# Kernel tuning notes

Hardware: AMD Instinct MI355X
Metric: run time of the kernel (lower is better)

The kernel has to match this reference:

```python
import jax, jax.numpy as jnp
import numpy as np

MAX_SEQ_LEN = 4096

def bigbird_block_rand_mask(from_seq_length, to_seq_length, from_block_size, to_block_size, num_rand_blocks, last_idx=-1):
    rand_attn = np.zeros((from_seq_length // from_block_size - 2, num_rand_blocks), dtype=np.int32)
    middle_seq = np.arange(1, to_seq_length // to_block_size - 1, dtype=np.int32)
    last = to_seq_length // to_block_size - 1
    if last_idx > 2 * to_block_size:
        last = last_idx // to_block_size - 1
    r = num_rand_blocks
    nfb = from_seq_length // from_block_size
    for i in range(1, nfb - 1):
        start = i - 2
        end = i
        if i == 1:
            rand_attn[i - 1, :] = np.random.permutation(middle_seq[2:last])[:r]
        elif i == 2:
            rand_attn[i - 1, :] = np.random.permutation(middle_seq[3:last])[:r]
        elif i == nfb - 3:
            rand_attn[i - 1, :] = np.random.permutation(middle_seq[:last])[:r]
        elif i == nfb - 2:
            rand_attn[i - 1, :] = np.random.permutation(middle_seq[:last])[:r]
        elif start > last:
            start = last
            rand_attn[i - 1, :] = np.random.permutation(middle_seq[:start])[:r]
        elif end + 1 == last:
            rand_attn[i - 1, :] = np.random.permutation(middle_seq[:start])[:r]
        else:
            rand_attn[i - 1, :] = np.random.permutation(np.concatenate((middle_seq[:start], middle_seq[end + 1:last])))[:r]
    return rand_attn

def full_bigbird_mask(from_seq_length, to_seq_length, from_block_size, to_block_size, rand_attn):
    attn_mask = np.zeros((MAX_SEQ_LEN, MAX_SEQ_LEN), dtype=np.int32)
    for i in range(1, from_seq_length // from_block_size - 1):
        attn_mask[i * from_block_size:(i + 1) * from_block_size, (i - 1) * to_block_size:(i + 2) * to_block_size] = 1
        for j in rand_attn[i - 1, :]:
            attn_mask[i * from_block_size:(i + 1) * from_block_size, j * to_block_size:(j + 1) * to_block_size] = 1
    attn_mask[:from_block_size, :] = 1
    attn_mask[:, :to_block_size] = 1
    attn_mask[:, -to_block_size:] = 1
    attn_mask[-from_block_size:, :] = 1
    return attn_mask[:from_seq_length, :to_seq_length].astype(bool)

def setup_inputs() -> dict:
    B, H, F, T, D = 2, 16, 1024, 1024, 64
    BS, R, SEED = 64, 3, 0
    np.random.seed(SEED)
    rand_attn = np.stack([
        bigbird_block_rand_mask(MAX_SEQ_LEN, MAX_SEQ_LEN, BS, BS, R, last_idx=1024)[:F // BS - 2]
        for _ in range(H)
    ], axis=0)
    mask = np.stack([full_bigbird_mask(F, T, BS, BS, rand_attn[h]) for h in range(H)], axis=0)
    attention_mask = jnp.asarray(mask[None].astype(np.float32))  # [1, H, F, T]
    key = jax.random.key(0)
    kq, kk, kv = jax.random.split(key, 3)
    return {
        'query_layer': jax.random.normal(kq, (B, H, F, D), dtype=jnp.float32),
        'key_layer': jax.random.normal(kk, (B, H, T, D), dtype=jnp.float32),
        'value_layer': jax.random.normal(kv, (B, H, T, D), dtype=jnp.float32),
        'attention_mask': attention_mask,
    }

def reference(query_layer, key_layer, value_layer, attention_mask):
    d = query_layer.shape[-1]
    scores = jnp.einsum('bnfh,bnth->bnft', query_layer, key_layer) * (1.0 / np.sqrt(float(d)))
    scores = scores + (1.0 - attention_mask) * -10000.0
    probs = jax.nn.softmax(scores, axis=-1)
    # [batch, from_seq, heads, size_per_head]
    return jnp.einsum('bnft,bnth->bfnh', probs, value_layer)
```

## Files before the change

### kernel.cpp

```cpp
#include <hip/hip_runtime.h>

typedef __attribute__((ext_vector_type(4))) float f32x4;
typedef __attribute__((ext_vector_type(8))) short bf16x8;
typedef _Float16 f16x8 __attribute__((ext_vector_type(8)));

#define MFMA16(a, b, c) __builtin_amdgcn_mfma_f32_16x16x32_f16((a), (b), (c), 0, 0, 0)
#define MFMABF(a, b, c) __builtin_amdgcn_mfma_f32_16x16x32_bf16((a), (b), (c), 0, 0, 0)

constexpr size_t TILE_FRAG_BYTES = 8192;
constexpr size_t NTILES = 512;
constexpr size_t ARR_S  = NTILES * TILE_FRAG_BYTES;
constexpr size_t WS_NEED = 2 * ARR_S;

__device__ __forceinline__ int swz_off(int row, int col) {
    return (row * 128 + col * 2) ^ ((row & 7) << 4);
}
__device__ __forceinline__ f16x8 ld_frag16(const char* tile, int row, int col) {
    return *(const f16x8*)(tile + swz_off(row, col));
}

__global__ __launch_bounds__(256) void bigbird_prepass(
    const float* __restrict__ K, const float* __restrict__ V,
    char* __restrict__ ws) {
    __shared__ float kf[64][66];
    __shared__ float vf[64][66];
    const int tile = blockIdx.x;
    const int tid  = threadIdx.x;
    const int row  = tid >> 2;
    const int c0   = (tid & 3) << 4;
    const float* Kt = K + (size_t)tile * 4096;
    const float* Vt = V + (size_t)tile * 4096;
    {
        const float* p = Kt + row * 64 + c0;
        f32x4 a = *(const f32x4*)p, bq = *(const f32x4*)(p + 4),
              c = *(const f32x4*)(p + 8), d = *(const f32x4*)(p + 12);
#pragma unroll
        for (int e = 0; e < 4; ++e) {
            kf[row][c0 + e] = a[e];      kf[row][c0 + 4 + e] = bq[e];
            kf[row][c0 + 8 + e] = c[e];  kf[row][c0 + 12 + e] = d[e];
        }
        const float* q = Vt + row * 64 + c0;
        f32x4 e0 = *(const f32x4*)q, e1 = *(const f32x4*)(q + 4),
              e2 = *(const f32x4*)(q + 8), e3 = *(const f32x4*)(q + 12);
#pragma unroll
        for (int e = 0; e < 4; ++e) {
            vf[row][c0 + e] = e0[e];     vf[row][c0 + 4 + e] = e1[e];
            vf[row][c0 + 8 + e] = e2[e]; vf[row][c0 + 12 + e] = e3[e];
        }
    }
    __syncthreads();
    f16x8* Ko = (f16x8*)(ws + (size_t)tile * TILE_FRAG_BYTES);
    f16x8* Vo = (f16x8*)(ws + ARR_S + (size_t)tile * TILE_FRAG_BYTES);
#pragma unroll
    for (int t = 0; t < 2; ++t) {
        int s = tid + t * 256;
        int f = s >> 6, lane = s & 63;
        int j = f >> 1, kk = f & 1;
        int l16 = lane & 15, g = lane >> 4;
        f16x8 kv, vv;
#pragma unroll
        for (int e = 0; e < 8; ++e) {
            kv[e] = (_Float16)kf[j * 16 + l16][kk * 32 + g * 8 + e];
            vv[e] = (_Float16)vf[kk * 32 + g * 8 + e][j * 16 + l16];
        }
        Ko[s] = kv;
        Vo[s] = vv;
    }
}

__global__ __launch_bounds__(256) void bigbird_main(
    const float* __restrict__ Q, const float* __restrict__ M,
    const char* __restrict__ ws, float* __restrict__ Out) {
    constexpr int H = 16, F = 1024, D = 64;

    __shared__ char p_sm[8192];
    __shared__ int flags[16];
    __shared__ int list[16];
    __shared__ int ncnt;

    const int i0  = blockIdx.x;
    const int xcd = i0 & 7;
    const int q0  = i0 >> 3;
    const int grp = xcd * 4 + (q0 >> 4);
    const int fb  = q0 & 15;
    const int b   = grp >> 4;
    const int h   = grp & 15;
    const int bh  = grp;

    const int tid  = threadIdx.x;
    const int lane = tid & 63;
    const int w    = tid >> 6;
    const int g    = lane >> 4;
    const int l16  = lane & 15;

    if (tid < 16)
        flags[tid] = (M[((size_t)(h * 1024 + fb * 64)) * 1024 + tid * 64] > 0.5f) ? 1 : 0;

    f16x8 qf[2];
    {
        const float* qr = Q + ((size_t)bh * F + fb * 64 + w * 16 + l16) * D;
#pragma unroll
        for (int kk = 0; kk < 2; ++kk) {
            const float* p = qr + kk * 32 + g * 8;
            f32x4 a = *(const f32x4*)p;
            f32x4 c = *(const f32x4*)(p + 4);
#pragma unroll
            for (int e = 0; e < 8; ++e)
                qf[kk][e] = (_Float16)((e < 4 ? a[e] : c[e - 4]) * 0.125f);
        }
    }
    __syncthreads();
    if (tid == 0) {
        int nn = 0;
        for (int t = 0; t < 16; ++t)
            if (flags[t]) list[nn++] = t;
        ncnt = nn;
    }
    __syncthreads();
    const int n = ncnt;

    f32x4 acc[4];
    float m_r[4], l_r[4];
#pragma unroll
    for (int j = 0; j < 4; ++j) acc[j] = f32x4{0.f, 0.f, 0.f, 0.f};
#pragma unroll
    for (int r = 0; r < 4; ++r) { m_r[r] = -1e30f; l_r[r] = 0.f; }

    const f16x8* Kbase = (const f16x8*)ws + (size_t)bh * 16 * 512;
    const f16x8* Vbase = (const f16x8*)(ws + ARR_S) + (size_t)bh * 16 * 512;

    for (int i = 0; i < n; ++i) {
        const int tb = list[i];
        const f16x8* Kf = Kbase + (size_t)tb * 512;
        const f16x8* Vf = Vbase + (size_t)tb * 512;

        f16x8 kfr[4][2], vfr[4][2];
#pragma unroll
        for (int j = 0; j < 4; ++j)
#pragma unroll
            for (int kk = 0; kk < 2; ++kk) {
                kfr[j][kk] = Kf[(j * 2 + kk) * 64 + lane];
                vfr[j][kk] = Vf[(j * 2 + kk) * 64 + lane];
            }

        f32x4 s[4];
#pragma unroll
        for (int j = 0; j < 4; ++j) {
            s[j] = f32x4{0.f, 0.f, 0.f, 0.f};
#pragma unroll
            for (int kk = 0; kk < 2; ++kk)
                s[j] = MFMA16(qf[kk], kfr[j][kk], s[j]);
        }

        float rmax[4];
#pragma unroll
        for (int r = 0; r < 4; ++r)
            rmax[r] = fmaxf(fmaxf(s[0][r], s[1][r]), fmaxf(s[2][r], s[3][r]));
#pragma unroll
        for (int off = 1; off < 16; off <<= 1)
#pragma unroll
            for (int r = 0; r < 4; ++r)
                rmax[r] = fmaxf(rmax[r], __shfl_xor(rmax[r], off, 64));
        float alpha[4], psum[4];
#pragma unroll
        for (int r = 0; r < 4; ++r) {
            float mn = fmaxf(m_r[r], rmax[r]);
            alpha[r] = __expf(m_r[r] - mn);
            m_r[r]   = mn;
            psum[r]  = 0.f;
        }
#pragma unroll
        for (int j = 0; j < 4; ++j)
#pragma unroll
            for (int r = 0; r < 4; ++r) {
                float pe = __expf(s[j][r] - m_r[r]);
                s[j][r] = pe;
                psum[r] += pe;
            }
#pragma unroll
        for (int off = 1; off < 16; off <<= 1)
#pragma unroll
            for (int r = 0; r < 4; ++r)
                psum[r] += __shfl_xor(psum[r], off, 64);
#pragma unroll
        for (int r = 0; r < 4; ++r)
            l_r[r] = l_r[r] * alpha[r] + psum[r];
#pragma unroll
        for (int j = 0; j < 4; ++j)
#pragma unroll
            for (int r = 0; r < 4; ++r)
                acc[j][r] *= alpha[r];

#pragma unroll
        for (int j = 0; j < 4; ++j)
#pragma unroll
            for (int r = 0; r < 4; ++r) {
                int row = w * 16 + g * 4 + r;
                *(_Float16*)(p_sm + swz_off(row, j * 16 + l16)) = (_Float16)s[j][r];
            }
        asm volatile("s_waitcnt lgkmcnt(0)" ::: "memory");
        __builtin_amdgcn_sched_barrier(0);

#pragma unroll
        for (int kk = 0; kk < 2; ++kk) {
            f16x8 pa = ld_frag16(p_sm, w * 16 + l16, kk * 32 + g * 8);
#pragma unroll
            for (int jd = 0; jd < 4; ++jd)
                acc[jd] = MFMA16(pa, vfr[jd][kk], acc[jd]);
        }
    }

#pragma unroll
    for (int r = 0; r < 4; ++r) {
        float inv = 1.0f / l_r[r];
        int f = fb * 64 + w * 16 + g * 4 + r;
        float* ob = Out + ((size_t)(b * F + f) * H + h) * D;
#pragma unroll
        for (int jd = 0; jd < 4; ++jd)
            ob[jd * 16 + l16] = acc[jd][r] * inv;
    }
}

__device__ __forceinline__ unsigned short f2bf(float x) {
    unsigned u = __builtin_bit_cast(unsigned, x);
    unsigned r = u + 0x7fffu + ((u >> 16) & 1u);
    return (unsigned short)(r >> 16);
}
__device__ __forceinline__ float bf2f(unsigned short h) {
    return __builtin_bit_cast(float, (unsigned)h << 16);
}
__device__ __forceinline__ bf16x8 ld_fragb(const char* tile, int row, int col) {
    return *(const bf16x8*)(tile + swz_off(row, col));
}
__device__ __forceinline__ void stage_rm_fb(const float* __restrict__ src,
                                            char* hi_t, char* lo_t, float scale) {
    const int tid = threadIdx.x;
    const int row = tid >> 2;
    const int c0  = (tid & 3) << 4;
    const float* p = src + row * 64 + c0;
    f32x4 vv[4] = { *(const f32x4*)(p), *(const f32x4*)(p + 4),
                    *(const f32x4*)(p + 8), *(const f32x4*)(p + 12) };
    bf16x8 h2[2], l2[2];
#pragma unroll
    for (int e = 0; e < 16; ++e) {
        float x = vv[e >> 2][e & 3] * scale;
        unsigned short hb = f2bf(x);
        unsigned short lb = f2bf(x - bf2f(hb));
        h2[e >> 3][e & 7] = (short)hb;
        l2[e >> 3][e & 7] = (short)lb;
    }
#pragma unroll
    for (int gi = 0; gi < 2; ++gi) {
        int off = swz_off(row, c0 + gi * 8);
        *(bf16x8*)(hi_t + off) = h2[gi];
        *(bf16x8*)(lo_t + off) = l2[gi];
    }
}
__device__ __forceinline__ void stage_tr_fb(const float* __restrict__ src,
                                            char* hi_t, char* lo_t) {
    const int tid = threadIdx.x;
    const int t  = tid >> 2;
    const int c0 = (tid & 3) << 4;
    const float* p = src + t * 64 + c0;
    f32x4 vv[4] = { *(const f32x4*)(p), *(const f32x4*)(p + 4),
                    *(const f32x4*)(p + 8), *(const f32x4*)(p + 12) };
#pragma unroll
    for (int e = 0; e < 16; ++e) {
        float x = vv[e >> 2][e & 3];
        unsigned short hb = f2bf(x);
        unsigned short lb = f2bf(x - bf2f(hb));
        int d = c0 + e;
        int off = (d * 128 + t * 2) ^ ((d & 7) << 4);
        *(unsigned short*)(hi_t + off) = hb;
        *(unsigned short*)(lo_t + off) = lb;
    }
}
__global__ __launch_bounds__(256) void bigbird_kernel_fb(
    const float* __restrict__ Q, const float* __restrict__ K,
    const float* __restrict__ V, const float* __restrict__ M,
    float* __restrict__ Out) {
    constexpr int H = 16, F = 1024, D = 64;
    __shared__ char kq_hi[8192];
    __shared__ char kq_lo[8192];
    __shared__ char vt_hi[8192];
    __shared__ char vt_lo[8192];
    __shared__ char p_sm[8192];
    __shared__ int flags[16];
    const int bid = blockIdx.x;
    const int fb  = bid & 15;
    const int h   = (bid >> 4) & 15;
    const int b   = bid >> 8;
    const int tid  = threadIdx.x;
    const int lane = tid & 63;
    const int w    = tid >> 6;
    const int g    = lane >> 4;
    const int l16  = lane & 15;
    if (tid < 16)
        flags[tid] = (M[(h * 1024 + fb * 64) * 1024 + tid * 64] > 0.5f) ? 1 : 0;
    const float* qb = Q + ((size_t)(b * H + h) * F + fb * 64) * D;
    stage_rm_fb(qb, kq_hi, kq_lo, 0.125f);
    __syncthreads();
    bf16x8 qh[2], ql[2];
#pragma unroll
    for (int kk = 0; kk < 2; ++kk) {
        qh[kk] = ld_fragb(kq_hi, w * 16 + l16, kk * 32 + g * 8);
        ql[kk] = ld_fragb(kq_lo, w * 16 + l16, kk * 32 + g * 8);
    }
    f32x4 acc[4];
    float m_r[4], l_r[4];
#pragma unroll
    for (int j = 0; j < 4; ++j) acc[j] = f32x4{0.f, 0.f, 0.f, 0.f};
#pragma unroll
    for (int r = 0; r < 4; ++r) { m_r[r] = -1e30f; l_r[r] = 0.f; }
    const float* kb = K + (size_t)(b * H + h) * 1024 * D;
    const float* vb = V + (size_t)(b * H + h) * 1024 * D;
    for (int tb = 0; tb < 16; ++tb) {
        if (!flags[tb]) continue;
        __syncthreads();
        stage_rm_fb(kb + tb * 64 * D, kq_hi, kq_lo, 1.0f);
        stage_tr_fb(vb + tb * 64 * D, vt_hi, vt_lo);
        __syncthreads();
        f32x4 s[4];
#pragma unroll
        for (int j = 0; j < 4; ++j) {
            s[j] = f32x4{0.f, 0.f, 0.f, 0.f};
#pragma unroll
            for (int kk = 0; kk < 2; ++kk) {
                bf16x8 bhf = ld_fragb(kq_hi, j * 16 + l16, kk * 32 + g * 8);
                bf16x8 blf = ld_fragb(kq_lo, j * 16 + l16, kk * 32 + g * 8);
                s[j] = MFMABF(qh[kk], bhf, s[j]);
                s[j] = MFMABF(qh[kk], blf, s[j]);
                s[j] = MFMABF(ql[kk], bhf, s[j]);
            }
        }
        float rmax[4];
#pragma unroll
        for (int r = 0; r < 4; ++r)
            rmax[r] = fmaxf(fmaxf(s[0][r], s[1][r]), fmaxf(s[2][r], s[3][r]));
#pragma unroll
        for (int off = 1; off < 16; off <<= 1)
#pragma unroll
            for (int r = 0; r < 4; ++r)
                rmax[r] = fmaxf(rmax[r], __shfl_xor(rmax[r], off, 64));
        float alpha[4], psum[4];
#pragma unroll
        for (int r = 0; r < 4; ++r) {
            float mn = fmaxf(m_r[r], rmax[r]);
            alpha[r] = __expf(m_r[r] - mn);
            m_r[r]   = mn;
            psum[r]  = 0.f;
        }
#pragma unroll
        for (int j = 0; j < 4; ++j)
#pragma unroll
            for (int r = 0; r < 4; ++r) {
                float pe = __expf(s[j][r] - m_r[r]);
                s[j][r] = pe;
                psum[r] += pe;
            }
#pragma unroll
        for (int off = 1; off < 16; off <<= 1)
#pragma unroll
            for (int r = 0; r < 4; ++r)
                psum[r] += __shfl_xor(psum[r], off, 64);
#pragma unroll
        for (int r = 0; r < 4; ++r)
            l_r[r] = l_r[r] * alpha[r] + psum[r];
#pragma unroll
        for (int j = 0; j < 4; ++j)
#pragma unroll
            for (int r = 0; r < 4; ++r)
                acc[j][r] *= alpha[r];
#pragma unroll
        for (int j = 0; j < 4; ++j)
#pragma unroll
            for (int r = 0; r < 4; ++r) {
                int row = w * 16 + g * 4 + r;
                *(unsigned short*)(p_sm + swz_off(row, j * 16 + l16)) = f2bf(s[j][r]);
            }
        __syncthreads();
#pragma unroll
        for (int kk = 0; kk < 2; ++kk) {
            bf16x8 pa = ld_fragb(p_sm, w * 16 + l16, kk * 32 + g * 8);
#pragma unroll
            for (int jd = 0; jd < 4; ++jd) {
                bf16x8 vh = ld_fragb(vt_hi, jd * 16 + l16, kk * 32 + g * 8);
                bf16x8 vl = ld_fragb(vt_lo, jd * 16 + l16, kk * 32 + g * 8);
                acc[jd] = MFMABF(pa, vh, acc[jd]);
                acc[jd] = MFMABF(pa, vl, acc[jd]);
            }
        }
    }
#pragma unroll
    for (int r = 0; r < 4; ++r) {
        float inv = 1.0f / l_r[r];
        int f = fb * 64 + w * 16 + g * 4 + r;
        float* ob = Out + ((size_t)(b * F + f) * H + h) * D;
#pragma unroll
        for (int jd = 0; jd < 4; ++jd)
            ob[jd * 16 + l16] = acc[jd][r] * inv;
    }
}

extern "C" void kernel_launch(void* const* d_in, const int* in_sizes, int n_in,
                              void* d_out, int out_size, void* d_ws, size_t ws_size,
                              hipStream_t stream) {
    const float* q = (const float*)d_in[0];
    const float* k = (const float*)d_in[1];
    const float* v = (const float*)d_in[2];
    const float* m = (const float*)d_in[3];
    float* out = (float*)d_out;
    if (ws_size >= WS_NEED) {
        bigbird_prepass<<<dim3(512), dim3(256), 0, stream>>>(k, v, (char*)d_ws);
        bigbird_main<<<dim3(512), dim3(256), 0, stream>>>(q, m, (const char*)d_ws, out);
    } else {
        bigbird_kernel_fb<<<dim3(512), dim3(256), 0, stream>>>(q, k, v, m, out);
    }
}
```

Before: 39.00 us.

## Split key blocks across wave pairs with split-softmax merge and smaller query tiles

The main kernel now handles 32 query rows per block instead of 64 and launches twice as many blocks. Within a block, two wave pairs each process alternate key blocks from the sparse list. Their partial softmax states are merged through shared memory with max and sum rescaling before the output is written. The prepass reads K fragments directly from global memory and only stages V through LDS for the transpose. This is meant to raise parallelism and occupancy for a small grid, at the cost of extra LDS traffic and two more barriers for the merge.

Result: no change. 39.08 us (+0.2%).

```diff
diff --git a/kernel.cpp b/kernel.cpp
--- a/kernel.cpp
+++ b/kernel.cpp
@@ -22,58 +22,66 @@
 __global__ __launch_bounds__(256) void bigbird_prepass(
     const float* __restrict__ K, const float* __restrict__ V,
     char* __restrict__ ws) {
-    __shared__ float kf[64][66];
     __shared__ float vf[64][66];
     const int tile = blockIdx.x;
     const int tid  = threadIdx.x;
-    const int row  = tid >> 2;
-    const int c0   = (tid & 3) << 4;
     const float* Kt = K + (size_t)tile * 4096;
     const float* Vt = V + (size_t)tile * 4096;
+    f16x8* Ko = (f16x8*)(ws + (size_t)tile * TILE_FRAG_BYTES);
+    f16x8* Vo = (f16x8*)(ws + ARR_S + (size_t)tile * TILE_FRAG_BYTES);
+
     {
-        const float* p = Kt + row * 64 + c0;
-        f32x4 a = *(const f32x4*)p, bq = *(const f32x4*)(p + 4),
-              c = *(const f32x4*)(p + 8), d = *(const f32x4*)(p + 12);
-#pragma unroll
-        for (int e = 0; e < 4; ++e) {
-            kf[row][c0 + e] = a[e];      kf[row][c0 + 4 + e] = bq[e];
-            kf[row][c0 + 8 + e] = c[e];  kf[row][c0 + 12 + e] = d[e];
-        }
-        const float* q = Vt + row * 64 + c0;
-        f32x4 e0 = *(const f32x4*)q, e1 = *(const f32x4*)(q + 4),
-              e2 = *(const f32x4*)(q + 8), e3 = *(const f32x4*)(q + 12);
+        const int row = tid >> 2;
+        const int c0  = (tid & 3) << 4;
+        const float* p = Vt + row * 64 + c0;
+        f32x4 e0 = *(const f32x4*)p,       e1 = *(const f32x4*)(p + 4),
+              e2 = *(const f32x4*)(p + 8), e3 = *(const f32x4*)(p + 12);
 #pragma unroll
         for (int e = 0; e < 4; ++e) {
             vf[row][c0 + e] = e0[e];     vf[row][c0 + 4 + e] = e1[e];
             vf[row][c0 + 8 + e] = e2[e]; vf[row][c0 + 12 + e] = e3[e];
         }
     }
-    __syncthreads();
-    f16x8* Ko = (f16x8*)(ws + (size_t)tile * TILE_FRAG_BYTES);
-    f16x8* Vo = (f16x8*)(ws + ARR_S + (size_t)tile * TILE_FRAG_BYTES);
 #pragma unroll
     for (int t = 0; t < 2; ++t) {
         int s = tid + t * 256;
         int f = s >> 6, lane = s & 63;
         int j = f >> 1, kk = f & 1;
         int l16 = lane & 15, g = lane >> 4;
-        f16x8 kv, vv;
-#pragma unroll
-        for (int e = 0; e < 8; ++e) {
-            kv[e] = (_Float16)kf[j * 16 + l16][kk * 32 + g * 8 + e];
+        const float* p = Kt + (j * 16 + l16) * 64 + kk * 32 + g * 8;
+        f32x4 a = *(const f32x4*)p;
+        f32x4 c = *(const f32x4*)(p + 4);
+        f16x8 kv;
+#pragma unroll
+        for (int e = 0; e < 4; ++e) {
+            kv[e]     = (_Float16)a[e];
+            kv[4 + e] = (_Float16)c[e];
+        }
+        Ko[s] = kv;
+    }
+    __syncthreads();
+#pragma unroll
+    for (int t = 0; t < 2; ++t) {
+        int s = tid + t * 256;
+        int f = s >> 6, lane = s & 63;
+        int j = f >> 1, kk = f & 1;
+        int l16 = lane & 15, g = lane >> 4;
+        f16x8 vv;
+#pragma unroll
+        for (int e = 0; e < 8; ++e)
             vv[e] = (_Float16)vf[kk * 32 + g * 8 + e][j * 16 + l16];
-        }
-        Ko[s] = kv;
         Vo[s] = vv;
     }
 }
 
-__global__ __launch_bounds__(256) void bigbird_main(
+__global__ __launch_bounds__(256, 4) void bigbird_main(
     const float* __restrict__ Q, const float* __restrict__ M,
     const char* __restrict__ ws, float* __restrict__ Out) {
     constexpr int H = 16, F = 1024, D = 64;
 
-    __shared__ char p_sm[8192];
+    __shared__ char  p_sm[4][2048];
+    __shared__ float O_sm[32][65];
+    __shared__ float m_sm[2][32], l_sm[2][32];
     __shared__ int flags[16];
     __shared__ int list[16];
     __shared__ int ncnt;
@@ -81,8 +89,8 @@
     const int i0  = blockIdx.x;
     const int xcd = i0 & 7;
     const int q0  = i0 >> 3;
-    const int grp = xcd * 4 + (q0 >> 4);
-    const int fb  = q0 & 15;
+    const int grp = xcd * 4 + (q0 >> 5);
+    const int sb  = q0 & 31;
     const int b   = grp >> 4;
     const int h   = grp & 15;
     const int bh  = grp;
@@ -90,15 +98,17 @@
     const int tid  = threadIdx.x;
     const int lane = tid & 63;
     const int w    = tid >> 6;
+    const int ws_  = w & 1;
+    const int wt   = w >> 1;
     const int g    = lane >> 4;
     const int l16  = lane & 15;
 
     if (tid < 16)
-        flags[tid] = (M[((size_t)(h * 1024 + fb * 64)) * 1024 + tid * 64] > 0.5f) ? 1 : 0;
+        flags[tid] = (M[((size_t)(h * 1024 + sb * 32)) * 1024 + tid * 64] > 0.5f) ? 1 : 0;
 
     f16x8 qf[2];
     {
-        const float* qr = Q + ((size_t)bh * F + fb * 64 + w * 16 + l16) * D;
+        const float* qr = Q + ((size_t)bh * F + sb * 32 + ws_ * 16 + l16) * D;
 #pragma unroll
         for (int kk = 0; kk < 2; ++kk) {
             const float* p = qr + kk * 32 + g * 8;
@@ -128,8 +138,9 @@
 
     const f16x8* Kbase = (const f16x8*)ws + (size_t)bh * 16 * 512;
     const f16x8* Vbase = (const f16x8*)(ws + ARR_S) + (size_t)bh * 16 * 512;
-
-    for (int i = 0; i < n; ++i) {
+    char* pw = p_sm[w];
+
+    for (int i = wt; i < n; i += 2) {
         const int tb = list[i];
         const f16x8* Kf = Kbase + (size_t)tb * 512;
         const f16x8* Vf = Vbase + (size_t)tb * 512;
@@ -194,30 +205,69 @@
 #pragma unroll
         for (int j = 0; j < 4; ++j)
 #pragma unroll
-            for (int r = 0; r < 4; ++r) {
-                int row = w * 16 + g * 4 + r;
-                *(_Float16*)(p_sm + swz_off(row, j * 16 + l16)) = (_Float16)s[j][r];
-            }
+            for (int r = 0; r < 4; ++r)
+                *(_Float16*)(pw + swz_off(g * 4 + r, j * 16 + l16)) = (_Float16)s[j][r];
         asm volatile("s_waitcnt lgkmcnt(0)" ::: "memory");
         __builtin_amdgcn_sched_barrier(0);
 
 #pragma unroll
         for (int kk = 0; kk < 2; ++kk) {
-            f16x8 pa = ld_frag16(p_sm, w * 16 + l16, kk * 32 + g * 8);
+            f16x8 pa = ld_frag16(pw, l16, kk * 32 + g * 8);
 #pragma unroll
             for (int jd = 0; jd < 4; ++jd)
                 acc[jd] = MFMA16(pa, vfr[jd][kk], acc[jd]);
         }
     }
 
+    if (l16 == 0) {
+#pragma unroll
+        for (int r = 0; r < 4; ++r) {
+            int row = ws_ * 16 + g * 4 + r;
+            m_sm[wt][row] = m_r[r];
+            l_sm[wt][row] = l_r[r];
+        }
+    }
+    __syncthreads();
+    float inv_l[4];
 #pragma unroll
     for (int r = 0; r < 4; ++r) {
-        float inv = 1.0f / l_r[r];
-        int f = fb * 64 + w * 16 + g * 4 + r;
+        int row = ws_ * 16 + g * 4 + r;
+        float m0 = m_sm[0][row], m1 = m_sm[1][row];
+        float mm = fmaxf(m0, m1);
+        float ll = l_sm[0][row] * __expf(m0 - mm) + l_sm[1][row] * __expf(m1 - mm);
+        inv_l[r] = 1.0f / ll;
+        float sc = __expf(m_r[r] - mm);
+#pragma unroll
+        for (int j = 0; j < 4; ++j) acc[j][r] *= sc;
+    }
+    if (wt == 0) {
+#pragma unroll
+        for (int j = 0; j < 4; ++j)
+#pragma unroll
+            for (int r = 0; r < 4; ++r)
+                O_sm[ws_ * 16 + g * 4 + r][j * 16 + l16] = acc[j][r];
+    }
+    __syncthreads();
+    if (wt == 1) {
+#pragma unroll
+        for (int j = 0; j < 4; ++j)
+#pragma unroll
+            for (int r = 0; r < 4; ++r)
+                O_sm[ws_ * 16 + g * 4 + r][j * 16 + l16] += acc[j][r];
+    }
+    __syncthreads();
+
+#pragma unroll
+    for (int r = 0; r < 4; ++r) {
+        int row = ws_ * 16 + g * 4 + r;
+        int f = sb * 32 + row;
+        float inv = inv_l[r];
         float* ob = Out + ((size_t)(b * F + f) * H + h) * D;
 #pragma unroll
-        for (int jd = 0; jd < 4; ++jd)
-            ob[jd * 16 + l16] = acc[jd][r] * inv;
+        for (int j2 = 0; j2 < 2; ++j2) {
+            int col = wt * 32 + j2 * 16 + l16;
+            ob[col] = O_sm[row][col] * inv;
+        }
     }
 }
 
@@ -284,7 +334,7 @@
     __shared__ char kq_lo[8192];
     __shared__ char vt_hi[8192];
     __shared__ char vt_lo[8192];
-    __shared__ char p_sm[8192];
+    __shared__ char p_smf[8192];
     __shared__ int flags[16];
     const int bid = blockIdx.x;
     const int fb  = bid & 15;
@@ -376,12 +426,12 @@
 #pragma unroll
             for (int r = 0; r < 4; ++r) {
                 int row = w * 16 + g * 4 + r;
-                *(unsigned short*)(p_sm + swz_off(row, j * 16 + l16)) = f2bf(s[j][r]);
+                *(unsigned short*)(p_smf + swz_off(row, j * 16 + l16)) = f2bf(s[j][r]);
             }
         __syncthreads();
 #pragma unroll
         for (int kk = 0; kk < 2; ++kk) {
-            bf16x8 pa = ld_fragb(p_sm, w * 16 + l16, kk * 32 + g * 8);
+            bf16x8 pa = ld_fragb(p_smf, w * 16 + l16, kk * 32 + g * 8);
 #pragma unroll
             for (int jd = 0; jd < 4; ++jd) {
                 bf16x8 vh = ld_fragb(vt_hi, jd * 16 + l16, kk * 32 + g * 8);
@@ -412,7 +462,7 @@
     float* out = (float*)d_out;
     if (ws_size >= WS_NEED) {
         bigbird_prepass<<<dim3(512), dim3(256), 0, stream>>>(k, v, (char*)d_ws);
-        bigbird_main<<<dim3(512), dim3(256), 0, stream>>>(q, m, (const char*)d_ws, out);
+        bigbird_main<<<dim3(1024), dim3(256), 0, stream>>>(q, m, (const char*)d_ws, out);
     } else {
         bigbird_kernel_fb<<<dim3(512), dim3(256), 0, stream>>>(q, k, v, m, out);
     }
```

## Double-buffer K/V fragments into LDS via async global_load_lds in main kernel

Applied to the files above, without the earlier changes.

The main kernel now stages each selected K/V tile into a double-buffered LDS region using global_load_lds, prefetching the next tile while computing the current one. Before, each wave loaded fragments directly from global memory into registers. The P scratch is split per wave, launch bounds now request 2 blocks per CU, and the prepass converts K straight from global memory without an LDS transpose. The price is an extra __syncthreads per iteration and more LDS use, which could limit occupancy.

New measurement: 44.82 us. 1.15x slower.

```diff
diff --git a/kernel.cpp b/kernel.cpp
--- a/kernel.cpp
+++ b/kernel.cpp
@@ -22,58 +22,65 @@
 __global__ __launch_bounds__(256) void bigbird_prepass(
     const float* __restrict__ K, const float* __restrict__ V,
     char* __restrict__ ws) {
-    __shared__ float kf[64][66];
     __shared__ float vf[64][66];
     const int tile = blockIdx.x;
     const int tid  = threadIdx.x;
-    const int row  = tid >> 2;
-    const int c0   = (tid & 3) << 4;
     const float* Kt = K + (size_t)tile * 4096;
     const float* Vt = V + (size_t)tile * 4096;
+    f16x8* Ko = (f16x8*)(ws + (size_t)tile * TILE_FRAG_BYTES);
+    f16x8* Vo = (f16x8*)(ws + ARR_S + (size_t)tile * TILE_FRAG_BYTES);
+
     {
-        const float* p = Kt + row * 64 + c0;
-        f32x4 a = *(const f32x4*)p, bq = *(const f32x4*)(p + 4),
-              c = *(const f32x4*)(p + 8), d = *(const f32x4*)(p + 12);
-#pragma unroll
-        for (int e = 0; e < 4; ++e) {
-            kf[row][c0 + e] = a[e];      kf[row][c0 + 4 + e] = bq[e];
-            kf[row][c0 + 8 + e] = c[e];  kf[row][c0 + 12 + e] = d[e];
-        }
-        const float* q = Vt + row * 64 + c0;
-        f32x4 e0 = *(const f32x4*)q, e1 = *(const f32x4*)(q + 4),
-              e2 = *(const f32x4*)(q + 8), e3 = *(const f32x4*)(q + 12);
+        const int row = tid >> 2;
+        const int c0  = (tid & 3) << 4;
+        const float* p = Vt + row * 64 + c0;
+        f32x4 e0 = *(const f32x4*)p,       e1 = *(const f32x4*)(p + 4),
+              e2 = *(const f32x4*)(p + 8), e3 = *(const f32x4*)(p + 12);
 #pragma unroll
         for (int e = 0; e < 4; ++e) {
             vf[row][c0 + e] = e0[e];     vf[row][c0 + 4 + e] = e1[e];
             vf[row][c0 + 8 + e] = e2[e]; vf[row][c0 + 12 + e] = e3[e];
         }
     }
-    __syncthreads();
-    f16x8* Ko = (f16x8*)(ws + (size_t)tile * TILE_FRAG_BYTES);
-    f16x8* Vo = (f16x8*)(ws + ARR_S + (size_t)tile * TILE_FRAG_BYTES);
 #pragma unroll
     for (int t = 0; t < 2; ++t) {
         int s = tid + t * 256;
         int f = s >> 6, lane = s & 63;
         int j = f >> 1, kk = f & 1;
         int l16 = lane & 15, g = lane >> 4;
-        f16x8 kv, vv;
-#pragma unroll
-        for (int e = 0; e < 8; ++e) {
-            kv[e] = (_Float16)kf[j * 16 + l16][kk * 32 + g * 8 + e];
+        const float* p = Kt + (j * 16 + l16) * 64 + kk * 32 + g * 8;
+        f32x4 a = *(const f32x4*)p;
+        f32x4 c = *(const f32x4*)(p + 4);
+        f16x8 kv;
+#pragma unroll
+        for (int e = 0; e < 4; ++e) {
+            kv[e]     = (_Float16)a[e];
+            kv[4 + e] = (_Float16)c[e];
+        }
+        Ko[s] = kv;
+    }
+    __syncthreads();
+#pragma unroll
+    for (int t = 0; t < 2; ++t) {
+        int s = tid + t * 256;
+        int f = s >> 6, lane = s & 63;
+        int j = f >> 1, kk = f & 1;
+        int l16 = lane & 15, g = lane >> 4;
+        f16x8 vv;
+#pragma unroll
+        for (int e = 0; e < 8; ++e)
             vv[e] = (_Float16)vf[kk * 32 + g * 8 + e][j * 16 + l16];
-        }
-        Ko[s] = kv;
         Vo[s] = vv;
     }
 }
 
-__global__ __launch_bounds__(256) void bigbird_main(
+__global__ __launch_bounds__(256, 2) void bigbird_main(
     const float* __restrict__ Q, const float* __restrict__ M,
     const char* __restrict__ ws, float* __restrict__ Out) {
     constexpr int H = 16, F = 1024, D = 64;
 
-    __shared__ char p_sm[8192];
+    __shared__ char fbuf[2][16384];
+    __shared__ char p_sm[4][2048];
     __shared__ int flags[16];
     __shared__ int list[16];
     __shared__ int ncnt;
@@ -126,30 +133,40 @@
 #pragma unroll
     for (int r = 0; r < 4; ++r) { m_r[r] = -1e30f; l_r[r] = 0.f; }
 
-    const f16x8* Kbase = (const f16x8*)ws + (size_t)bh * 16 * 512;
-    const f16x8* Vbase = (const f16x8*)(ws + ARR_S) + (size_t)bh * 16 * 512;
+    const char* wsK = ws + (size_t)bh * 16 * TILE_FRAG_BYTES;
+    const char* wsV = wsK + ARR_S;
+    char* pw = p_sm[w];
+
+    auto stage = [&](int bufi, int tb) {
+        const char* Kt = wsK + (size_t)tb * TILE_FRAG_BYTES;
+        const char* Vt = wsV + (size_t)tb * TILE_FRAG_BYTES;
+        char* dst = fbuf[bufi] + w * 1024;
+#pragma unroll
+        for (int c = 0; c < 4; ++c) {
+            const char* src = (c < 2 ? Kt + c * 4096 : Vt + (c - 2) * 4096) + tid * 16;
+            __builtin_amdgcn_global_load_lds(
+                (const __attribute__((address_space(1))) void*)src,
+                (__attribute__((address_space(3))) void*)(dst + c * 4096), 16, 0, 0);
+        }
+    };
+
+    if (n > 0) stage(0, list[0]);
 
     for (int i = 0; i < n; ++i) {
-        const int tb = list[i];
-        const f16x8* Kf = Kbase + (size_t)tb * 512;
-        const f16x8* Vf = Vbase + (size_t)tb * 512;
-
-        f16x8 kfr[4][2], vfr[4][2];
-#pragma unroll
-        for (int j = 0; j < 4; ++j)
-#pragma unroll
-            for (int kk = 0; kk < 2; ++kk) {
-                kfr[j][kk] = Kf[(j * 2 + kk) * 64 + lane];
-                vfr[j][kk] = Vf[(j * 2 + kk) * 64 + lane];
-            }
+        __syncthreads();
+        if (i + 1 < n) stage((i + 1) & 1, list[i + 1]);
+        const char* Kb = fbuf[i & 1];
+        const char* Vb = fbuf[i & 1] + 8192;
 
         f32x4 s[4];
 #pragma unroll
         for (int j = 0; j < 4; ++j) {
             s[j] = f32x4{0.f, 0.f, 0.f, 0.f};
 #pragma unroll
-            for (int kk = 0; kk < 2; ++kk)
-                s[j] = MFMA16(qf[kk], kfr[j][kk], s[j]);
+            for (int kk = 0; kk < 2; ++kk) {
+                f16x8 kf = *(const f16x8*)(Kb + (j * 2 + kk) * 1024 + lane * 16);
+                s[j] = MFMA16(qf[kk], kf, s[j]);
+            }
         }
 
         float rmax[4];
@@ -194,19 +211,19 @@
 #pragma unroll
         for (int j = 0; j < 4; ++j)
 #pragma unroll
-            for (int r = 0; r < 4; ++r) {
-                int row = w * 16 + g * 4 + r;
-                *(_Float16*)(p_sm + swz_off(row, j * 16 + l16)) = (_Float16)s[j][r];
-            }
+            for (int r = 0; r < 4; ++r)
+                *(_Float16*)(pw + swz_off(g * 4 + r, j * 16 + l16)) = (_Float16)s[j][r];
         asm volatile("s_waitcnt lgkmcnt(0)" ::: "memory");
         __builtin_amdgcn_sched_barrier(0);
 
 #pragma unroll
         for (int kk = 0; kk < 2; ++kk) {
-            f16x8 pa = ld_frag16(p_sm, w * 16 + l16, kk * 32 + g * 8);
-#pragma unroll
-            for (int jd = 0; jd < 4; ++jd)
-                acc[jd] = MFMA16(pa, vfr[jd][kk], acc[jd]);
+            f16x8 pa = ld_frag16(pw, l16, kk * 32 + g * 8);
+#pragma unroll
+            for (int jd = 0; jd < 4; ++jd) {
+                f16x8 vfr = *(const f16x8*)(Vb + (jd * 2 + kk) * 1024 + lane * 16);
+                acc[jd] = MFMA16(pa, vfr, acc[jd]);
+            }
         }
     }
 
@@ -284,7 +301,7 @@
     __shared__ char kq_lo[8192];
     __shared__ char vt_hi[8192];
     __shared__ char vt_lo[8192];
-    __shared__ char p_sm[8192];
+    __shared__ char p_smf[8192];
     __shared__ int flags[16];
     const int bid = blockIdx.x;
     const int fb  = bid & 15;
@@ -376,12 +393,12 @@
 #pragma unroll
             for (int r = 0; r < 4; ++r) {
                 int row = w * 16 + g * 4 + r;
-                *(unsigned short*)(p_sm + swz_off(row, j * 16 + l16)) = f2bf(s[j][r]);
+                *(unsigned short*)(p_smf + swz_off(row, j * 16 + l16)) = f2bf(s[j][r]);
             }
         __syncthreads();
 #pragma unroll
         for (int kk = 0; kk < 2; ++kk) {
-            bf16x8 pa = ld_fragb(p_sm, w * 16 + l16, kk * 32 + g * 8);
+            bf16x8 pa = ld_fragb(p_smf, w * 16 + l16, kk * 32 + g * 8);
 #pragma unroll
             for (int jd = 0; jd < 4; ++jd) {
                 bf16x8 vh = ld_fragb(vt_hi, jd * 16 + l16, kk * 32 + g * 8);
```
